# Performance work log

Hardware: AMD Instinct MI355X
Metric: run time of the kernel (lower is better)

Reference implementation:

```python
import jax, jax.numpy as jnp
import numpy as np

B, SQ, SK, D, H = 8, 1024, 1024, 768, 12
HD = D // H  # 64


def setup_inputs() -> dict:
    key = jax.random.key(0)
    ks = jax.random.split(key, 6)
    s = 0.02
    return {
        "hidden_states": jax.random.normal(ks[0], (B, SQ, D), jnp.float32),
        "context": jax.random.normal(ks[1], (B, SK, D), jnp.float32),
        "attention_mask": jnp.zeros((B, 1, 1, SK), jnp.float32),
        "Wq": jax.random.normal(ks[2], (D, D), jnp.float32) * s,
        "bq": jnp.zeros((D,), jnp.float32),
        "Wk": jax.random.normal(ks[3], (D, D), jnp.float32) * s,
        "bk": jnp.zeros((D,), jnp.float32),
        "Wv": jax.random.normal(ks[4], (D, D), jnp.float32) * s,
        "bv": jnp.zeros((D,), jnp.float32),
    }


def _split_heads(x):
    # [B, S, D] -> [B, H, S, HD]
    b, s, _ = x.shape
    return x.reshape(b, s, H, HD).transpose(0, 2, 1, 3)


def reference(hidden_states, context, attention_mask, Wq, bq, Wk, bk, Wv, bv):
    q = _split_heads(hidden_states @ Wq + bq)   # [B,H,SQ,HD]
    k = _split_heads(context @ Wk + bk)         # [B,H,SK,HD]
    v = _split_heads(context @ Wv + bv)         # [B,H,SK,HD]
    scores = jnp.einsum("bhqd,bhkd->bhqk", q, k) / jnp.sqrt(jnp.float32(HD))
    scores = scores + attention_mask            # broadcast [B,1,1,SK]
    probs = jax.nn.softmax(scores, axis=-1)     # dropout p=0 -> identity
    ctx = jnp.einsum("bhqk,bhkd->bhqd", probs, v)
    return ctx.transpose(0, 2, 1, 3).reshape(hidden_states.shape[0], -1, H * HD)
```

## Files before the change

kernel.cpp:

```cpp
#include <hip/hip_runtime.h>
#include <hip/hip_bf16.h>
#include <cstdint>

#define B_  8
#define SQ_ 1024
#define SK_ 1024
#define D_  768
#define H_  12
#define HD_ 64

typedef __attribute__((ext_vector_type(8))) short s16x8;
typedef __attribute__((ext_vector_type(4))) float f32x4;

__device__ __forceinline__ float bf2f(ushort u) {
    union { uint32_t i; float f; } v; v.i = ((uint32_t)u) << 16; return v.f;
}
__device__ __forceinline__ ushort f2bf(float f) {
    __hip_bfloat16 h = __float2bfloat16(f);
    union { __hip_bfloat16 h; ushort u; } v; v.h = h; return v.u;
}
__device__ __forceinline__ uint32_t pk32(float a, float b) {
    return (uint32_t)f2bf(a) | ((uint32_t)f2bf(b) << 16);
}

__global__ void convX(const float4* __restrict__ src, ushort* __restrict__ dst, int n4) {
    int i = blockIdx.x * blockDim.x + threadIdx.x;
    int stride = gridDim.x * blockDim.x;
    for (; i < n4; i += stride) {
        float4 v = src[i];
        ushort4 o = { f2bf(v.x), f2bf(v.y), f2bf(v.z), f2bf(v.w) };
        *reinterpret_cast<ushort4*>(dst + (size_t)i * 4) = o;
    }
}

__global__ void convWT(const float* __restrict__ W, ushort* __restrict__ WT) {
    __shared__ float t[32][33];
    int k0 = blockIdx.x * 32, n0 = blockIdx.y * 32;
    int tx = threadIdx.x & 31, ty = threadIdx.x >> 5;
#pragma unroll
    for (int rr = 0; rr < 4; ++rr)
        t[ty + 8 * rr][tx] = W[(size_t)(k0 + ty + 8 * rr) * D_ + n0 + tx];
    __syncthreads();
#pragma unroll
    for (int rr = 0; rr < 4; ++rr)
        WT[(size_t)(n0 + ty + 8 * rr) * D_ + k0 + tx] = f2bf(t[tx][ty + 8 * rr]);
}

#define GL16(g, l)                                                                     \
    __builtin_amdgcn_global_load_lds((const __attribute__((address_space(1))) void*)(g), \
                                     (__attribute__((address_space(3))) void*)(l), 16, 0, 0)

__global__ __launch_bounds__(256) void gemm_qkv(
    const ushort* __restrict__ hb, const ushort* __restrict__ cb,
    const ushort* __restrict__ wqt, const ushort* __restrict__ wkt, const ushort* __restrict__ wvt,
    const float* __restrict__ bq, const float* __restrict__ bk, const float* __restrict__ bv,
    ushort* __restrict__ qout, ushort* __restrict__ kout, ushort* __restrict__ vtout)
{
    const int z = blockIdx.z;
    const ushort* A    = (z == 0) ? hb : cb;
    const ushort* Wt   = (z == 0) ? wqt : (z == 1) ? wkt : wvt;
    const float*  bias = (z == 0) ? bq  : (z == 1) ? bk  : bv;

    __shared__ ushort As[128 * 32];
    __shared__ ushort Bs[128 * 32];

    const int tid = threadIdx.x;
    const int w = tid >> 6, l = tid & 63;
    const int g = l >> 4, c = l & 15;
    const int wr = w >> 1, wc = w & 1;
    const int m0 = blockIdx.x * 128;
    const int n0 = blockIdx.y * 128;

    f32x4 acc[4][4];
#pragma unroll
    for (int mi = 0; mi < 4; ++mi)
#pragma unroll
        for (int ni = 0; ni < 4; ++ni) acc[mi][ni] = (f32x4){0.f, 0.f, 0.f, 0.f};

    for (int kt = 0; kt < D_ / 32; ++kt) {
        __syncthreads();
#pragma unroll
        for (int j = 0; j < 2; ++j) {
            int cc = (j * 4 + w) * 64 + l;
            int row = cc >> 2, c8 = cc & 3;
            const ushort* ga = A  + (size_t)(m0 + row) * D_ + kt * 32 + c8 * 8;
            GL16(ga, (char*)As + (size_t)(j * 4 + w) * 1024);
            const ushort* gb = Wt + (size_t)(n0 + row) * D_ + kt * 32 + c8 * 8;
            GL16(gb, (char*)Bs + (size_t)(j * 4 + w) * 1024);
        }
        __syncthreads();

        s16x8 af[4], bfr[4];
#pragma unroll
        for (int mi = 0; mi < 4; ++mi)
            af[mi] = *(const s16x8*)&As[(wr * 64 + mi * 16 + c) * 32 + g * 8];
#pragma unroll
        for (int ni = 0; ni < 4; ++ni)
            bfr[ni] = *(const s16x8*)&Bs[(wc * 64 + ni * 16 + c) * 32 + g * 8];
#pragma unroll
        for (int mi = 0; mi < 4; ++mi)
#pragma unroll
            for (int ni = 0; ni < 4; ++ni)
                acc[mi][ni] = __builtin_amdgcn_mfma_f32_16x16x32_bf16(af[mi], bfr[ni], acc[mi][ni], 0, 0, 0);
    }

    if (z < 2) {
        ushort* Out = (z == 0) ? qout : kout;
#pragma unroll
        for (int ni = 0; ni < 4; ++ni) {
            int ncol = n0 + wc * 64 + ni * 16 + c;
            float bv_ = bias[ncol];
#pragma unroll
            for (int mi = 0; mi < 4; ++mi) {
#pragma unroll
                for (int r = 0; r < 4; ++r) {
                    int mrow = m0 + wr * 64 + mi * 16 + 4 * g + r;
                    Out[(size_t)mrow * D_ + ncol] = f2bf(acc[mi][ni][r] + bv_);
                }
            }
        }
    } else {
#pragma unroll
        for (int ni = 0; ni < 4; ++ni) {
            int ncol = n0 + wc * 64 + ni * 16 + c;
            float bv_ = bias[ncol];
            int hh = ncol >> 6, dd = ncol & 63;
#pragma unroll
            for (int mi = 0; mi < 4; ++mi) {
                int mrow = m0 + wr * 64 + mi * 16 + 4 * g;
                int bb = mrow >> 10, ss = mrow & 1023;
                ushort4 pk;
                pk.x = f2bf(acc[mi][ni][0] + bv_);
                pk.y = f2bf(acc[mi][ni][1] + bv_);
                pk.z = f2bf(acc[mi][ni][2] + bv_);
                pk.w = f2bf(acc[mi][ni][3] + bv_);
                *reinterpret_cast<ushort4*>(vtout + (size_t)((bb * H_ + hh) * HD_ + dd) * SK_ + ss) = pk;
            }
        }
    }
}

__global__ __launch_bounds__(256) void attn(
    const ushort* __restrict__ Qb, const ushort* __restrict__ Kb, const ushort* __restrict__ VT,
    const float* __restrict__ amask, float* __restrict__ out)
{
    __shared__ ushort Ks[2][64 * 64];
    __shared__ ushort Vs[2][64 * 64];
    __shared__ float  Ms[1024];

    const int tid = threadIdx.x;
    const int w = tid >> 6, l = tid & 63;
    const int g = l >> 4, c = l & 15;
    const int q0 = blockIdx.x * 64;
    const int h  = blockIdx.y;
    const int b  = blockIdx.z;
    const int xsw = (c & 7) << 4;
    const int lane0 = c + 16 * ((2 * g) & 3);
    const int lane1 = c + 16 * ((2 * g + 1) & 3);
    const bool hi_ = (g >= 2);
    const float L2E = 1.44269504f;

#pragma unroll
    for (int i = 0; i < 4; ++i) Ms[tid + 256 * i] = amask[b * SK_ + tid + 256 * i];

    s16x8 qf[2];
#pragma unroll
    for (int kk = 0; kk < 2; ++kk) {
        const ushort* gq = Qb + (size_t)(b * SQ_ + q0 + w * 16 + c) * D_ + h * HD_ + kk * 32 + g * 8;
        s16x8 v = *(const s16x8*)gq;
#pragma unroll
        for (int i = 0; i < 8; ++i) v[i] = (short)f2bf(bf2f((ushort)v[i]) * 0.125f);
        qf[kk] = v;
    }

    const int row0 = tid >> 3, c8 = tid & 7;
    const int ldsoff = row0 * 128 + ((c8 * 16) ^ ((row0 & 7) << 4));
    const ushort* kp = Kb + (size_t)(b * SK_ + row0) * D_ + h * HD_ + c8 * 8;
    const ushort* vp = VT + (size_t)((b * H_ + h) * HD_ + row0) * SK_ + c8 * 8;

    {
        uint4 k0 = *(const uint4*)kp, k1 = *(const uint4*)(kp + 32 * D_);
        uint4 v0 = *(const uint4*)vp, v1 = *(const uint4*)(vp + 32 * SK_);
        *(uint4*)((char*)Ks[0] + ldsoff) = k0;
        *(uint4*)((char*)Ks[0] + ldsoff + 4096) = k1;
        *(uint4*)((char*)Vs[0] + ldsoff) = v0;
        *(uint4*)((char*)Vs[0] + ldsoff + 4096) = v1;
        kp += 64 * D_; vp += 64;
    }
    __syncthreads();

    f32x4 o[4];
#pragma unroll
    for (int nn = 0; nn < 4; ++nn) o[nn] = (f32x4){0.f, 0.f, 0.f, 0.f};
    float m_run = -INFINITY, ps = 0.f;

#define TILE(CUR, NXT, T)                                                              \
    {                                                                                  \
                                 \
        uint4 nk0 = *(const uint4*)kp;                                                 \
        uint4 nk1 = *(const uint4*)(kp + 32 * D_);                                     \
        uint4 nv0 = *(const uint4*)vp;                                                 \
        uint4 nv1 = *(const uint4*)(vp + 32 * SK_);                                    \
        if ((T) < 14) { kp += 64 * D_; vp += 64; }                                     \
                             \
        float sv[4][4];                                                                \
        _Pragma("unroll")                                                              \
        for (int n = 0; n < 4; ++n) {                                                  \
            f32x4 s = (f32x4){0.f, 0.f, 0.f, 0.f};                                     \
            _Pragma("unroll")                                                          \
            for (int kk = 0; kk < 2; ++kk) {                                           \
                const s16x8 kf = *(const s16x8*)((const char*)Ks[CUR] +                \
                    (16 * n + c) * 128 + ((kk * 64 + g * 16) ^ xsw));                  \
                s = __builtin_amdgcn_mfma_f32_16x16x32_bf16(kf, qf[kk], s, 0, 0, 0);   \
            }                                                                          \
            const f32x4 mk = *(const f32x4*)&Ms[(T) * 64 + n * 16 + g * 4];            \
            _Pragma("unroll")                                                          \
            for (int r = 0; r < 4; ++r) sv[n][r] = s[r] + mk[r];                       \
        }                                                                              \
                                     \
        float pmax = sv[0][0];                                                         \
        _Pragma("unroll")                                                              \
        for (int n = 0; n < 4; ++n)                                                    \
            _Pragma("unroll")                                                          \
            for (int r = 0; r < 4; ++r) pmax = fmaxf(pmax, sv[n][r]);                  \
        if (__any(pmax > m_run + 8.f)) {                                               \
            float mf = fmaxf(pmax, __shfl_xor(pmax, 16));                              \
            mf = fmaxf(mf, __shfl_xor(mf, 32));                                        \
            float mn = fmaxf(m_run, mf);                                               \
            float alpha = exp2f((m_run - mn) * L2E);                                   \
            m_run = mn; ps *= alpha;                                                   \
            float ar0 = __shfl(alpha, 4 * g), ar1 = __shfl(alpha, 4 * g + 1);          \
            float ar2 = __shfl(alpha, 4 * g + 2), ar3 = __shfl(alpha, 4 * g + 3);      \
            _Pragma("unroll")                                                          \
            for (int nn = 0; nn < 4; ++nn) {                                           \
                o[nn][0] *= ar0; o[nn][1] *= ar1; o[nn][2] *= ar2; o[nn][3] *= ar3;    \
            }                                                                          \
        }                                                                              \
                                          \
        uint32_t pk[4][2];                                                             \
        _Pragma("unroll")                                                              \
        for (int n = 0; n < 4; ++n) {                                                  \
            float p0 = exp2f((sv[n][0] - m_run) * L2E);                                \
            float p1 = exp2f((sv[n][1] - m_run) * L2E);                                \
            float p2 = exp2f((sv[n][2] - m_run) * L2E);                                \
            float p3 = exp2f((sv[n][3] - m_run) * L2E);                                \
            ps += (p0 + p1) + (p2 + p3);                                               \
            pk[n][0] = pk32(p0, p1); pk[n][1] = pk32(p2, p3);                          \
        }                                                                              \
         \
        s16x8 pa0, pa1;                                                                \
        {                                                                              \
            union { uint32_t u[4]; s16x8 v; } ua, ub;                                  \
            uint32_t a0 = __shfl((int)pk[0][0], lane0), b0 = __shfl((int)pk[1][0], lane0); \
            uint32_t a1 = __shfl((int)pk[0][1], lane0), b1 = __shfl((int)pk[1][1], lane0); \
            uint32_t a2 = __shfl((int)pk[0][0], lane1), b2 = __shfl((int)pk[1][0], lane1); \
            uint32_t a3 = __shfl((int)pk[0][1], lane1), b3 = __shfl((int)pk[1][1], lane1); \
            ua.u[0] = hi_ ? b0 : a0; ua.u[1] = hi_ ? b1 : a1;                          \
            ua.u[2] = hi_ ? b2 : a2; ua.u[3] = hi_ ? b3 : a3;                          \
            uint32_t c0 = __shfl((int)pk[2][0], lane0), d0 = __shfl((int)pk[3][0], lane0); \
            uint32_t c1 = __shfl((int)pk[2][1], lane0), d1 = __shfl((int)pk[3][1], lane0); \
            uint32_t c2 = __shfl((int)pk[2][0], lane1), d2 = __shfl((int)pk[3][0], lane1); \
            uint32_t c3 = __shfl((int)pk[2][1], lane1), d3 = __shfl((int)pk[3][1], lane1); \
            ub.u[0] = hi_ ? d0 : c0; ub.u[1] = hi_ ? d1 : c1;                          \
            ub.u[2] = hi_ ? d2 : c2; ub.u[3] = hi_ ? d3 : c3;                          \
            pa0 = ua.v; pa1 = ub.v;                                                    \
        }                                                                              \
                                                                       \
        _Pragma("unroll")                                                              \
        for (int nn = 0; nn < 4; ++nn) {                                               \
            const s16x8 vf0 = *(const s16x8*)((const char*)Vs[CUR] +                   \
                (16 * nn + c) * 128 + ((g * 16) ^ xsw));                               \
            o[nn] = __builtin_amdgcn_mfma_f32_16x16x32_bf16(pa0, vf0, o[nn], 0, 0, 0); \
            const s16x8 vf1 = *(const s16x8*)((const char*)Vs[CUR] +                   \
                (16 * nn + c) * 128 + ((64 + g * 16) ^ xsw));                          \
            o[nn] = __builtin_amdgcn_mfma_f32_16x16x32_bf16(pa1, vf1, o[nn], 0, 0, 0); \
        }                                                                              \
                       \
        *(uint4*)((char*)Ks[NXT] + ldsoff) = nk0;                                      \
        *(uint4*)((char*)Ks[NXT] + ldsoff + 4096) = nk1;                               \
        *(uint4*)((char*)Vs[NXT] + ldsoff) = nv0;                                      \
        *(uint4*)((char*)Vs[NXT] + ldsoff + 4096) = nv1;                               \
        __syncthreads();                                                               \
    }

    for (int tt = 0; tt < 8; ++tt) {
        TILE(0, 1, 2 * tt)
        TILE(1, 0, 2 * tt + 1)
    }
#undef TILE

    ps += __shfl_xor(ps, 16);
    ps += __shfl_xor(ps, 32);
    float invc = 1.f / ps;
    float ir0 = __shfl(invc, 4 * g), ir1 = __shfl(invc, 4 * g + 1);
    float ir2 = __shfl(invc, 4 * g + 2), ir3 = __shfl(invc, 4 * g + 3);
#pragma unroll
    for (int nn = 0; nn < 4; ++nn) {
        float* op = out + (size_t)(b * SQ_ + q0 + w * 16 + 4 * g) * D_ + h * HD_ + 16 * nn + c;
        op[0]      = o[nn][0] * ir0;
        op[D_]     = o[nn][1] * ir1;
        op[2 * D_] = o[nn][2] * ir2;
        op[3 * D_] = o[nn][3] * ir3;
    }
}

extern "C" void kernel_launch(void* const* d_in, const int* in_sizes, int n_in,
                              void* d_out, int out_size, void* d_ws, size_t ws_size,
                              hipStream_t stream) {
    (void)in_sizes; (void)n_in; (void)out_size; (void)ws_size;
    const float* hidden  = (const float*)d_in[0];
    const float* context = (const float*)d_in[1];
    const float* amask   = (const float*)d_in[2];
    const float* Wq = (const float*)d_in[3];
    const float* bq = (const float*)d_in[4];
    const float* Wk = (const float*)d_in[5];
    const float* bk = (const float*)d_in[6];
    const float* Wv = (const float*)d_in[7];
    const float* bv = (const float*)d_in[8];
    float* out = (float*)d_out;

    char* ws = (char*)d_ws;
    ushort* hb  = (ushort*)(ws);
    ushort* cb  = (ushort*)(ws + 12582912);
    ushort* wqt = (ushort*)(ws + 25165824);
    ushort* wkt = (ushort*)(ws + 26345472);
    ushort* wvt = (ushort*)(ws + 27525120);
    ushort* qb  = (ushort*)(ws + 28704768);
    ushort* kb  = (ushort*)(ws + 41287680);
    ushort* vt  = (ushort*)(ws + 53870592);

    int n4 = (B_ * SQ_ * D_) / 4;
    convX<<<2048, 256, 0, stream>>>((const float4*)hidden, hb, n4);
    convX<<<2048, 256, 0, stream>>>((const float4*)context, cb, n4);
    dim3 gw(24, 24);
    convWT<<<gw, 256, 0, stream>>>(Wq, wqt);
    convWT<<<gw, 256, 0, stream>>>(Wk, wkt);
    convWT<<<gw, 256, 0, stream>>>(Wv, wvt);
    gemm_qkv<<<dim3(64, 6, 3), 256, 0, stream>>>(hb, cb, wqt, wkt, wvt, bq, bk, bv, qb, kb, vt);
    attn<<<dim3(16, 12, 8), 256, 0, stream>>>(qb, kb, vt, amask, out);
}
```

Before: 237.2 us.

## Restructure attention kernel around 32x32x16 MFMA with 64 queries per wave

Rewrites the attention kernel to use 32x32x16 bf16 MFMA instructions. Each wave now handles 64 query rows as two 32-row slices, and blocks shrink to 128 threads covering 128 queries. The mask is folded into the MFMA accumulator init, exp uses the hardware exp2 builtin, and the P-matrix relayout uses two xor-32 shuffles instead of many indexed shuffles. The aim is to halve K/V LDS traffic per query and cut shuffle and VALU overhead. In exchange it uses more registers per thread (launch bounds 128,2) and launches fewer blocks.

Measured after the change: 234.7 us. Within noise of the previous version (-1.1%).

```diff
diff --git a/kernel.cpp b/kernel.cpp
--- a/kernel.cpp
+++ b/kernel.cpp
@@ -11,6 +11,7 @@
 
 typedef __attribute__((ext_vector_type(8))) short s16x8;
 typedef __attribute__((ext_vector_type(4))) float f32x4;
+typedef __attribute__((ext_vector_type(16))) float f32x16;
 
 __device__ __forceinline__ float bf2f(ushort u) {
     union { uint32_t i; float f; } v; v.i = ((uint32_t)u) << 16; return v.f;
@@ -21,6 +22,19 @@
 }
 __device__ __forceinline__ uint32_t pk32(float a, float b) {
     return (uint32_t)f2bf(a) | ((uint32_t)f2bf(b) << 16);
+}
+__device__ __forceinline__ float fexp2(float x) {
+#if __has_builtin(__builtin_amdgcn_exp2f)
+    return __builtin_amdgcn_exp2f(x);
+#else
+    return exp2f(x);
+#endif
+}
+__device__ __forceinline__ void xch(uint32_t a, uint32_t b, bool lo, uint32_t& x, uint32_t& y) {
+    uint32_t bx = (uint32_t)__shfl_xor((int)b, 32);
+    uint32_t ax = (uint32_t)__shfl_xor((int)a, 32);
+    x = lo ? a : bx;
+    y = lo ? ax : b;
 }
 
 __global__ void convX(const float4* __restrict__ src, ushort* __restrict__ dst, int n4) {
@@ -140,7 +154,55 @@
     }
 }
 
-__global__ __launch_bounds__(256) void attn(
+#define MFMA32(a, b, c) __builtin_amdgcn_mfma_f32_32x32x16_bf16(a, b, c, 0, 0, 0)
+
+__device__ __forceinline__ void proc_qs(f32x16 sa, float& m_run, float& ps,
+                                        f32x16& o0, f32x16& o1,
+                                        const s16x8 v0a, const s16x8 v1a,
+                                        const s16x8 v0b, const s16x8 v1b,
+                                        const int hi, const bool lo)
+{
+    const float L2E = 1.44269504f;
+    float a0 = fmaxf(fmaxf(sa[0], sa[1]), fmaxf(sa[2], sa[3]));
+    float a1 = fmaxf(fmaxf(sa[4], sa[5]), fmaxf(sa[6], sa[7]));
+    float a2 = fmaxf(fmaxf(sa[8], sa[9]), fmaxf(sa[10], sa[11]));
+    float a3 = fmaxf(fmaxf(sa[12], sa[13]), fmaxf(sa[14], sa[15]));
+    float pmax = fmaxf(fmaxf(a0, a1), fmaxf(a2, a3));
+    if (__any(pmax > m_run + 8.f)) {
+        float mf = fmaxf(pmax, __shfl_xor(pmax, 32));
+        float mn = fmaxf(m_run, mf);
+        float alpha = fexp2((m_run - mn) * L2E);
+        m_run = mn; ps *= alpha;
+#pragma unroll
+        for (int r = 0; r < 16; ++r) {
+            float ar = __shfl(alpha, (r & 3) + 8 * (r >> 2) + 4 * hi);
+            o0[r] *= ar; o1[r] *= ar;
+        }
+    }
+    float ml = m_run * L2E;
+    float p[16];
+#pragma unroll
+    for (int r = 0; r < 16; ++r) p[r] = fexp2(sa[r] * L2E - ml);
+    ps += (((p[0] + p[1]) + (p[2] + p[3])) + ((p[4] + p[5]) + (p[6] + p[7]))) +
+          (((p[8] + p[9]) + (p[10] + p[11])) + ((p[12] + p[13]) + (p[14] + p[15])));
+    uint32_t cc[8];
+#pragma unroll
+    for (int j = 0; j < 8; ++j) cc[j] = pk32(p[2 * j], p[2 * j + 1]);
+    uint32_t d0, d1, d2, d3, e0, e1, e2, e3;
+    xch(cc[0], cc[2], lo, d0, d2);
+    xch(cc[1], cc[3], lo, d1, d3);
+    xch(cc[4], cc[6], lo, e0, e2);
+    xch(cc[5], cc[7], lo, e1, e3);
+    union { uint32_t u[4]; s16x8 v; } ua, ub;
+    ua.u[0] = d0; ua.u[1] = d1; ua.u[2] = d2; ua.u[3] = d3;
+    ub.u[0] = e0; ub.u[1] = e1; ub.u[2] = e2; ub.u[3] = e3;
+    o0 = MFMA32(ua.v, v0a, o0);
+    o0 = MFMA32(ub.v, v1a, o0);
+    o1 = MFMA32(ua.v, v0b, o1);
+    o1 = MFMA32(ub.v, v1b, o1);
+}
+
+__global__ __launch_bounds__(128, 2) void attn(
     const ushort* __restrict__ Qb, const ushort* __restrict__ Kb, const ushort* __restrict__ VT,
     const float* __restrict__ amask, float* __restrict__ out)
 {
@@ -149,29 +211,29 @@
     __shared__ float  Ms[1024];
 
     const int tid = threadIdx.x;
-    const int w = tid >> 6, l = tid & 63;
-    const int g = l >> 4, c = l & 15;
-    const int q0 = blockIdx.x * 64;
-    const int h  = blockIdx.y;
-    const int b  = blockIdx.z;
-    const int xsw = (c & 7) << 4;
-    const int lane0 = c + 16 * ((2 * g) & 3);
-    const int lane1 = c + 16 * ((2 * g + 1) & 3);
-    const bool hi_ = (g >= 2);
-    const float L2E = 1.44269504f;
-
-#pragma unroll
-    for (int i = 0; i < 4; ++i) Ms[tid + 256 * i] = amask[b * SK_ + tid + 256 * i];
-
-    s16x8 qf[2];
-#pragma unroll
-    for (int kk = 0; kk < 2; ++kk) {
-        const ushort* gq = Qb + (size_t)(b * SQ_ + q0 + w * 16 + c) * D_ + h * HD_ + kk * 32 + g * 8;
-        s16x8 v = *(const s16x8*)gq;
-#pragma unroll
-        for (int i = 0; i < 8; ++i) v[i] = (short)f2bf(bf2f((ushort)v[i]) * 0.125f);
-        qf[kk] = v;
-    }
+    const int w   = tid >> 6;
+    const int l   = tid & 63;
+    const int hi  = l >> 5;
+    const int l31 = l & 31;
+    const bool lo = (hi == 0);
+    const int swz = (l31 & 7) << 4;
+    const int q0  = blockIdx.x * 128 + w * 64;
+    const int h = blockIdx.y, b = blockIdx.z;
+
+    ((float4*)Ms)[tid]       = ((const float4*)(amask + b * SK_))[tid];
+    ((float4*)Ms)[tid + 128] = ((const float4*)(amask + b * SK_))[tid + 128];
+
+    s16x8 qf[2][4];
+#pragma unroll
+    for (int qs = 0; qs < 2; ++qs)
+#pragma unroll
+        for (int s = 0; s < 4; ++s) {
+            const ushort* gq = Qb + (size_t)(b * SQ_ + q0 + qs * 32 + l31) * D_ + h * HD_ + s * 16 + hi * 8;
+            s16x8 v = *(const s16x8*)gq;
+#pragma unroll
+            for (int i = 0; i < 8; ++i) v[i] = (short)f2bf(bf2f((ushort)v[i]) * 0.125f);
+            qf[qs][s] = v;
+        }
 
     const int row0 = tid >> 3, c8 = tid & 7;
     const int ldsoff = row0 * 128 + ((c8 * 16) ^ ((row0 & 7) << 4));
@@ -179,107 +241,73 @@
     const ushort* vp = VT + (size_t)((b * H_ + h) * HD_ + row0) * SK_ + c8 * 8;
 
     {
-        uint4 k0 = *(const uint4*)kp, k1 = *(const uint4*)(kp + 32 * D_);
-        uint4 v0 = *(const uint4*)vp, v1 = *(const uint4*)(vp + 32 * SK_);
-        *(uint4*)((char*)Ks[0] + ldsoff) = k0;
-        *(uint4*)((char*)Ks[0] + ldsoff + 4096) = k1;
-        *(uint4*)((char*)Vs[0] + ldsoff) = v0;
-        *(uint4*)((char*)Vs[0] + ldsoff + 4096) = v1;
+#pragma unroll
+        for (int i = 0; i < 4; ++i) {
+            *(uint4*)((char*)Ks[0] + ldsoff + 2048 * i) = *(const uint4*)(kp + i * 16 * D_);
+            *(uint4*)((char*)Vs[0] + ldsoff + 2048 * i) = *(const uint4*)(vp + i * 16 * SK_);
+        }
         kp += 64 * D_; vp += 64;
     }
     __syncthreads();
 
-    f32x4 o[4];
-#pragma unroll
-    for (int nn = 0; nn < 4; ++nn) o[nn] = (f32x4){0.f, 0.f, 0.f, 0.f};
-    float m_run = -INFINITY, ps = 0.f;
+    f32x16 o[2][2];
+#pragma unroll
+    for (int qs = 0; qs < 2; ++qs)
+#pragma unroll
+        for (int db = 0; db < 2; ++db)
+#pragma unroll
+            for (int r = 0; r < 16; ++r) o[qs][db][r] = 0.f;
+    float m_run[2] = { -INFINITY, -INFINITY };
+    float ps[2] = { 0.f, 0.f };
 
 #define TILE(CUR, NXT, T)                                                              \
     {                                                                                  \
-                                 \
-        uint4 nk0 = *(const uint4*)kp;                                                 \
-        uint4 nk1 = *(const uint4*)(kp + 32 * D_);                                     \
-        uint4 nv0 = *(const uint4*)vp;                                                 \
-        uint4 nv1 = *(const uint4*)(vp + 32 * SK_);                                    \
+        uint4 nk0 = *(const uint4*)(kp);                                               \
+        uint4 nk1 = *(const uint4*)(kp + 16 * D_);                                     \
+        uint4 nk2 = *(const uint4*)(kp + 32 * D_);                                     \
+        uint4 nk3 = *(const uint4*)(kp + 48 * D_);                                     \
+        uint4 nv0 = *(const uint4*)(vp);                                               \
+        uint4 nv1 = *(const uint4*)(vp + 16 * SK_);                                    \
+        uint4 nv2 = *(const uint4*)(vp + 32 * SK_);                                    \
+        uint4 nv3 = *(const uint4*)(vp + 48 * SK_);                                    \
         if ((T) < 14) { kp += 64 * D_; vp += 64; }                                     \
-                             \
-        float sv[4][4];                                                                \
         _Pragma("unroll")                                                              \
-        for (int n = 0; n < 4; ++n) {                                                  \
-            f32x4 s = (f32x4){0.f, 0.f, 0.f, 0.f};                                     \
+        for (int blk = 0; blk < 2; ++blk) {                                            \
+            const int kvb = (T) * 64 + blk * 32;                                       \
+            union { f32x4 q[4]; f32x16 v; } mku;                                       \
             _Pragma("unroll")                                                          \
-            for (int kk = 0; kk < 2; ++kk) {                                           \
-                const s16x8 kf = *(const s16x8*)((const char*)Ks[CUR] +                \
-                    (16 * n + c) * 128 + ((kk * 64 + g * 16) ^ xsw));                  \
-                s = __builtin_amdgcn_mfma_f32_16x16x32_bf16(kf, qf[kk], s, 0, 0, 0);   \
-            }                                                                          \
-            const f32x4 mk = *(const f32x4*)&Ms[(T) * 64 + n * 16 + g * 4];            \
+            for (int t = 0; t < 4; ++t)                                                \
+                mku.q[t] = *(const f32x4*)&Ms[kvb + 4 * hi + 8 * t];                   \
+            s16x8 kfr[4];                                                              \
             _Pragma("unroll")                                                          \
-            for (int r = 0; r < 4; ++r) sv[n][r] = s[r] + mk[r];                       \
-        }                                                                              \
-                                     \
-        float pmax = sv[0][0];                                                         \
-        _Pragma("unroll")                                                              \
-        for (int n = 0; n < 4; ++n)                                                    \
+            for (int s = 0; s < 4; ++s)                                                \
+                kfr[s] = *(const s16x8*)((const char*)Ks[CUR] + (blk * 32 + l31) * 128 \
+                                         + ((s * 32 + hi * 16) ^ swz));                \
+            s16x8 vfr[2][2];                                                           \
             _Pragma("unroll")                                                          \
-            for (int r = 0; r < 4; ++r) pmax = fmaxf(pmax, sv[n][r]);                  \
-        if (__any(pmax > m_run + 8.f)) {                                               \
-            float mf = fmaxf(pmax, __shfl_xor(pmax, 16));                              \
-            mf = fmaxf(mf, __shfl_xor(mf, 32));                                        \
-            float mn = fmaxf(m_run, mf);                                               \
-            float alpha = exp2f((m_run - mn) * L2E);                                   \
-            m_run = mn; ps *= alpha;                                                   \
-            float ar0 = __shfl(alpha, 4 * g), ar1 = __shfl(alpha, 4 * g + 1);          \
-            float ar2 = __shfl(alpha, 4 * g + 2), ar3 = __shfl(alpha, 4 * g + 3);      \
+            for (int sl = 0; sl < 2; ++sl)                                             \
+                _Pragma("unroll")                                                      \
+                for (int db = 0; db < 2; ++db)                                         \
+                    vfr[sl][db] = *(const s16x8*)((const char*)Vs[CUR] +               \
+                        (db * 32 + l31) * 128 + ((blk * 64 + sl * 32 + hi * 16) ^ swz)); \
             _Pragma("unroll")                                                          \
-            for (int nn = 0; nn < 4; ++nn) {                                           \
-                o[nn][0] *= ar0; o[nn][1] *= ar1; o[nn][2] *= ar2; o[nn][3] *= ar3;    \
+            for (int qs = 0; qs < 2; ++qs) {                                           \
+                f32x16 sa = MFMA32(kfr[0], qf[qs][0], mku.v);                          \
+                sa = MFMA32(kfr[1], qf[qs][1], sa);                                    \
+                sa = MFMA32(kfr[2], qf[qs][2], sa);                                    \
+                sa = MFMA32(kfr[3], qf[qs][3], sa);                                    \
+                proc_qs(sa, m_run[qs], ps[qs], o[qs][0], o[qs][1],                     \
+                        vfr[0][0], vfr[1][0], vfr[0][1], vfr[1][1], hi, lo);           \
             }                                                                          \
         }                                                                              \
-                                          \
-        uint32_t pk[4][2];                                                             \
-        _Pragma("unroll")                                                              \
-        for (int n = 0; n < 4; ++n) {                                                  \
-            float p0 = exp2f((sv[n][0] - m_run) * L2E);                                \
-            float p1 = exp2f((sv[n][1] - m_run) * L2E);                                \
-            float p2 = exp2f((sv[n][2] - m_run) * L2E);                                \
-            float p3 = exp2f((sv[n][3] - m_run) * L2E);                                \
-            ps += (p0 + p1) + (p2 + p3);                                               \
-            pk[n][0] = pk32(p0, p1); pk[n][1] = pk32(p2, p3);                          \
-        }                                                                              \
-         \
-        s16x8 pa0, pa1;                                                                \
-        {                                                                              \
-            union { uint32_t u[4]; s16x8 v; } ua, ub;                                  \
-            uint32_t a0 = __shfl((int)pk[0][0], lane0), b0 = __shfl((int)pk[1][0], lane0); \
-            uint32_t a1 = __shfl((int)pk[0][1], lane0), b1 = __shfl((int)pk[1][1], lane0); \
-            uint32_t a2 = __shfl((int)pk[0][0], lane1), b2 = __shfl((int)pk[1][0], lane1); \
-            uint32_t a3 = __shfl((int)pk[0][1], lane1), b3 = __shfl((int)pk[1][1], lane1); \
-            ua.u[0] = hi_ ? b0 : a0; ua.u[1] = hi_ ? b1 : a1;                          \
-            ua.u[2] = hi_ ? b2 : a2; ua.u[3] = hi_ ? b3 : a3;                          \
-            uint32_t c0 = __shfl((int)pk[2][0], lane0), d0 = __shfl((int)pk[3][0], lane0); \
-            uint32_t c1 = __shfl((int)pk[2][1], lane0), d1 = __shfl((int)pk[3][1], lane0); \
-            uint32_t c2 = __shfl((int)pk[2][0], lane1), d2 = __shfl((int)pk[3][0], lane1); \
-            uint32_t c3 = __shfl((int)pk[2][1], lane1), d3 = __shfl((int)pk[3][1], lane1); \
-            ub.u[0] = hi_ ? d0 : c0; ub.u[1] = hi_ ? d1 : c1;                          \
-            ub.u[2] = hi_ ? d2 : c2; ub.u[3] = hi_ ? d3 : c3;                          \
-            pa0 = ua.v; pa1 = ub.v;                                                    \
-        }                                                                              \
-                                                                       \
-        _Pragma("unroll")                                                              \
-        for (int nn = 0; nn < 4; ++nn) {                                               \
-            const s16x8 vf0 = *(const s16x8*)((const char*)Vs[CUR] +                   \
-                (16 * nn + c) * 128 + ((g * 16) ^ xsw));                               \
-            o[nn] = __builtin_amdgcn_mfma_f32_16x16x32_bf16(pa0, vf0, o[nn], 0, 0, 0); \
-            const s16x8 vf1 = *(const s16x8*)((const char*)Vs[CUR] +                   \
-                (16 * nn + c) * 128 + ((64 + g * 16) ^ xsw));                          \
-            o[nn] = __builtin_amdgcn_mfma_f32_16x16x32_bf16(pa1, vf1, o[nn], 0, 0, 0); \
-        }                                                                              \
-                       \
-        *(uint4*)((char*)Ks[NXT] + ldsoff) = nk0;                                      \
-        *(uint4*)((char*)Ks[NXT] + ldsoff + 4096) = nk1;                               \
-        *(uint4*)((char*)Vs[NXT] + ldsoff) = nv0;                                      \
-        *(uint4*)((char*)Vs[NXT] + ldsoff + 4096) = nv1;                               \
+        *(uint4*)((char*)Ks[NXT] + ldsoff)        = nk0;                               \
+        *(uint4*)((char*)Ks[NXT] + ldsoff + 2048) = nk1;                               \
+        *(uint4*)((char*)Ks[NXT] + ldsoff + 4096) = nk2;                               \
+        *(uint4*)((char*)Ks[NXT] + ldsoff + 6144) = nk3;                               \
+        *(uint4*)((char*)Vs[NXT] + ldsoff)        = nv0;                               \
+        *(uint4*)((char*)Vs[NXT] + ldsoff + 2048) = nv1;                               \
+        *(uint4*)((char*)Vs[NXT] + ldsoff + 4096) = nv2;                               \
+        *(uint4*)((char*)Vs[NXT] + ldsoff + 6144) = nv3;                               \
         __syncthreads();                                                               \
     }
 
@@ -289,18 +317,18 @@
     }
 #undef TILE
 
-    ps += __shfl_xor(ps, 16);
-    ps += __shfl_xor(ps, 32);
-    float invc = 1.f / ps;
-    float ir0 = __shfl(invc, 4 * g), ir1 = __shfl(invc, 4 * g + 1);
-    float ir2 = __shfl(invc, 4 * g + 2), ir3 = __shfl(invc, 4 * g + 3);
-#pragma unroll
-    for (int nn = 0; nn < 4; ++nn) {
-        float* op = out + (size_t)(b * SQ_ + q0 + w * 16 + 4 * g) * D_ + h * HD_ + 16 * nn + c;
-        op[0]      = o[nn][0] * ir0;
-        op[D_]     = o[nn][1] * ir1;
-        op[2 * D_] = o[nn][2] * ir2;
-        op[3 * D_] = o[nn][3] * ir3;
+#pragma unroll
+    for (int qs = 0; qs < 2; ++qs) {
+        float pf = ps[qs] + __shfl_xor(ps[qs], 32);
+        float inv = 1.f / pf;
+#pragma unroll
+        for (int r = 0; r < 16; ++r) {
+            int qr = (r & 3) + 8 * (r >> 2) + 4 * hi;
+            float iv = __shfl(inv, qr);
+            float* op = out + (size_t)(b * SQ_ + q0 + qs * 32 + qr) * D_ + h * HD_ + l31;
+            op[0]  = o[qs][0][r] * iv;
+            op[32] = o[qs][1][r] * iv;
+        }
     }
 }
 
@@ -337,5 +365,5 @@
     convWT<<<gw, 256, 0, stream>>>(Wk, wkt);
     convWT<<<gw, 256, 0, stream>>>(Wv, wvt);
     gemm_qkv<<<dim3(64, 6, 3), 256, 0, stream>>>(hb, cb, wqt, wkt, wvt, bq, bk, bv, qb, kb, vt);
-    attn<<<dim3(16, 12, 8), 256, 0, stream>>>(qb, kb, vt, amask, out);
-}
+    attn<<<dim3(8, 12, 8), 128, 0, stream>>>(qb, kb, vt, amask, out);
+}
```
